# Kernel optimization log

Measured on AMD Instinct MI355X. Metric: run time of the kernel, lower is better.

The kernel has to match this reference:

```python
import jax, jax.numpy as jnp
import numpy as np

S, T, H = 5120, 1024, 512
DL, DT, DC, DU = 512, 32, 64, 64
D = DL + DT + DC  # 608 rnn input size
LOC, TIM, CLU, UID = 50000, 48, 100, 10000


def setup_inputs() -> dict:
    key = jax.random.key(0)
    ks = jax.random.split(key, 20)
    r = lambda k, shape, s=0.02: (jax.random.normal(k, shape, dtype=jnp.float32) * s)
    return {
        "loc": jax.random.randint(ks[0], (S,), 0, LOC),
        "tim": jax.random.randint(ks[1], (S,), 0, TIM),
        "cluster": jax.random.randint(ks[2], (S,), 0, CLU),
        "uid": jax.random.randint(ks[3], (1,), 0, UID),
        "target_len": T,
        "emb_loc": r(ks[4], (LOC, DL)),
        "emb_tim": r(ks[5], (TIM, DT)),
        "emb_cluster": r(ks[6], (CLU, DC)),
        "emb_uid": r(ks[7], (UID, DU)),
        "enc_Wih": r(ks[8], (4 * H, D)),
        "enc_Whh": r(ks[9], (4 * H, H)),
        "enc_bih": jnp.zeros((4 * H,), jnp.float32),
        "enc_bhh": jnp.zeros((4 * H,), jnp.float32),
        "dec_Wih": r(ks[10], (4 * H, D)),
        "dec_Whh": r(ks[11], (4 * H, H)),
        "dec_bih": jnp.zeros((4 * H,), jnp.float32),
        "dec_bhh": jnp.zeros((4 * H,), jnp.float32),
        "fcW": r(ks[12], (LOC, 2 * H + DU)),
        "fcb": jnp.zeros((LOC,), jnp.float32),
    }


def _lstm(x, Wih, Whh, bih, bhh):
    # x: [S, D]; PyTorch LSTM gate order i, f, g, o
    h0 = jnp.zeros((H,), x.dtype)

    def step(carry, xt):
        h, c = carry
        g = xt @ Wih.T + bih + h @ Whh.T + bhh
        i, f, gg, o = jnp.split(g, 4)
        c = jax.nn.sigmoid(f) * c + jax.nn.sigmoid(i) * jnp.tanh(gg)
        h = jax.nn.sigmoid(o) * jnp.tanh(c)
        return (h, c), h

    _, hs = jax.lax.scan(step, (h0, h0), x)
    return hs  # [S, H]


def reference(loc, tim, cluster, uid, target_len, emb_loc, emb_tim, emb_cluster,
              emb_uid, enc_Wih, enc_Whh, enc_bih, enc_bhh, dec_Wih, dec_Whh,
              dec_bih, dec_bhh, fcW, fcb):
    # embed and concat; dropout is identity in eval mode
    x = jnp.concatenate([emb_loc[loc], emb_tim[tim], emb_cluster[cluster]], axis=-1)  # [S, D]
    hidden_history = _lstm(x[:-target_len], enc_Wih, enc_Whh, enc_bih, enc_bhh)  # [S-T, H]
    hidden_state = _lstm(x[-target_len:], dec_Wih, dec_Whh, dec_bih, dec_bhh)   # [T, H]
    # 'dot' attention: the O(T*Sh) python loop of scalar dots == one GEMM
    attn = jax.nn.softmax(hidden_state @ hidden_history.T, axis=-1)  # [T, S-T]
    context = attn @ hidden_history  # [T, H]
    uid_emb = jnp.broadcast_to(emb_uid[uid], (target_len, DU))  # repeat(target_len, 1)
    out = jnp.concatenate([hidden_state, context, uid_emb], axis=1)  # [T, 2H+DU]
    y = out @ fcW.T + fcb  # [T, LOC]
    return jax.nn.log_softmax(y, axis=-1)
```

## Files before the change

kernel.cpp:

```cpp
#include <hip/hip_runtime.h>

typedef unsigned short u16;
typedef unsigned int u32;
typedef unsigned long long u64;
typedef __attribute__((ext_vector_type(8))) short short8;
typedef __attribute__((ext_vector_type(4))) float f32x4;

__device__ __forceinline__ u16 f2bf(float f) {
    u32 u = __float_as_uint(f);
    u32 r = (u + 0x7fffu + ((u >> 16) & 1u)) >> 16;
    return (u16)r;
}
__device__ __forceinline__ float bfl(u32 u) { return __uint_as_float(u << 16); }
__device__ __forceinline__ float bfh(u32 u) { return __uint_as_float(u & 0xffff0000u); }
__device__ __forceinline__ u32 pk2(float a, float b) {
    return (u32)f2bf(a) | ((u32)f2bf(b) << 16);
}

#define S_TOT 5120
#define T_DEC 1024
#define S_ENC 4096
#define HDIM 512
#define DDIM 608
#define G4 2048
#define NLOC 50000
#define KFC 1088

__global__ void k_init(u64* he, u64* hd) {
    int i = blockIdx.x * 256 + threadIdx.x;
    if (i < 512) { he[i] = 0ull; hd[i] = 0ull; }
}

__global__ void k_bias(const float* a, const float* b, const float* c, const float* d,
                       float* be, float* bd) {
    int i = blockIdx.x * 256 + threadIdx.x;
    if (i < G4) { be[i] = a[i] + b[i]; bd[i] = c[i] + d[i]; }
}

__global__ __launch_bounds__(256) void k_embed(const int* __restrict__ loc, const int* __restrict__ tim,
    const int* __restrict__ clu, const float* __restrict__ el, const float* __restrict__ et,
    const float* __restrict__ ec, u16* __restrict__ xb) {
    const int s = blockIdx.x;
    const int ls = loc[s], lt = tim[s], lc = clu[s];
    for (int c = threadIdx.x; c < DDIM; c += 256) {
        float v;
        if (c < 512)       v = el[(size_t)ls * 512 + c];
        else if (c < 544)  v = et[lt * 32 + (c - 512)];
        else               v = ec[lc * 64 + (c - 544)];
        xb[(size_t)s * DDIM + c] = f2bf(v);
    }
}

template <bool BF32>
__global__ __launch_bounds__(256) void gemm_bt(
    const u16* __restrict__ A, const void* __restrict__ Bv, float* __restrict__ C,
    const float* __restrict__ bias, int N, int K, int lda, int ldb, int ldc) {
    __shared__ u16 As[128][40];
    __shared__ u16 Bs[128][40];
    const int tid = threadIdx.x;
    const int bn = blockIdx.x, bm = blockIdx.y;
    const int wave = tid >> 6, lane = tid & 63;
    const int quad = lane >> 4, l16 = lane & 15;
    const int wm = (wave & 1) << 6, wn = (wave >> 1) << 6;
    const int rq = tid >> 2, q4 = tid & 3;

    f32x4 acc[4][4] = {};

    const u16* Arow0 = A + (size_t)(bm * 128 + rq) * lda + q4 * 8;
    const u16* Arow1 = Arow0 + (size_t)64 * lda;

    const int rb0 = bn * 128 + rq, rb1 = rb0 + 64;
    const bool okb0 = rb0 < N, okb1 = rb1 < N;
    const float* Bf0 = nullptr; const float* Bf1 = nullptr;
    const u16* Bh0 = nullptr; const u16* Bh1 = nullptr;
    if constexpr (BF32) {
        const float* Bf = (const float*)Bv;
        Bf0 = Bf + (size_t)rb0 * ldb + q4 * 8;
        Bf1 = Bf + (size_t)rb1 * ldb + q4 * 8;
    } else {
        const u16* Bh = (const u16*)Bv;
        Bh0 = Bh + (size_t)rb0 * ldb + q4 * 8;
        Bh1 = Bh + (size_t)rb1 * ldb + q4 * 8;
    }

    uint4 a0, a1, bh0, bh1;
    float4 f00, f01, f10, f11;
    const float4 fz = make_float4(0.f, 0.f, 0.f, 0.f);
    auto fetch = [&](int k0) {
        a0 = *(const uint4*)(Arow0 + k0);
        a1 = *(const uint4*)(Arow1 + k0);
        if constexpr (BF32) {
            f00 = okb0 ? *(const float4*)(Bf0 + k0) : fz;
            f01 = okb0 ? *(const float4*)(Bf0 + k0 + 4) : fz;
            f10 = okb1 ? *(const float4*)(Bf1 + k0) : fz;
            f11 = okb1 ? *(const float4*)(Bf1 + k0 + 4) : fz;
        } else {
            bh0 = *(const uint4*)(Bh0 + k0);
            bh1 = *(const uint4*)(Bh1 + k0);
        }
    };
    fetch(0);
    for (int k0 = 0; k0 < K; k0 += 32) {
        __syncthreads();
        *(uint4*)&As[rq][q4 * 8] = a0;
        *(uint4*)&As[rq + 64][q4 * 8] = a1;
        if constexpr (BF32) {
            uint4 t0, t1;
            t0.x = pk2(f00.x, f00.y); t0.y = pk2(f00.z, f00.w);
            t0.z = pk2(f01.x, f01.y); t0.w = pk2(f01.z, f01.w);
            t1.x = pk2(f10.x, f10.y); t1.y = pk2(f10.z, f10.w);
            t1.z = pk2(f11.x, f11.y); t1.w = pk2(f11.z, f11.w);
            *(uint4*)&Bs[rq][q4 * 8] = t0;
            *(uint4*)&Bs[rq + 64][q4 * 8] = t1;
        } else {
            *(uint4*)&Bs[rq][q4 * 8] = bh0;
            *(uint4*)&Bs[rq + 64][q4 * 8] = bh1;
        }
        __syncthreads();
        if (k0 + 32 < K) fetch(k0 + 32);
        short8 af[4], bf[4];
#pragma unroll
        for (int i = 0; i < 4; i++) af[i] = *(const short8*)&As[wm + 16 * i + l16][quad * 8];
#pragma unroll
        for (int j = 0; j < 4; j++) bf[j] = *(const short8*)&Bs[wn + 16 * j + l16][quad * 8];
#pragma unroll
        for (int i = 0; i < 4; i++)
#pragma unroll
            for (int j = 0; j < 4; j++)
                acc[i][j] = __builtin_amdgcn_mfma_f32_16x16x32_bf16(af[i], bf[j], acc[i][j], 0, 0, 0);
    }
#pragma unroll
    for (int j = 0; j < 4; j++) {
        int c0 = bn * 128 + wn + 16 * j + l16;
        if (c0 >= N) continue;
        float bv = bias ? bias[c0] : 0.f;
#pragma unroll
        for (int i = 0; i < 4; i++) {
            int r0 = bm * 128 + wm + 16 * i + quad * 4;
#pragma unroll
            for (int rg = 0; rg < 4; rg++)
                C[(size_t)(r0 + rg) * ldc + c0] = acc[i][j][rg] + bv;
        }
    }
}

__global__ __launch_bounds__(256) void k_lstm(
    const float* __restrict__ Whh_e, const float* __restrict__ Whh_d,
    const float* __restrict__ XW,
    u64* __restrict__ hbc_e, u64* __restrict__ hbc_d,
    u16* __restrict__ Hh, u16* __restrict__ HhT, u16* __restrict__ OutA) {
    __shared__ u16 Wl[32][520];
    __shared__ float hbuf[512];
    __shared__ float gbuf[32];
    __shared__ float cbuf[8];
    const int tid = threadIdx.x;
    const bool enc = (blockIdx.x < 64);
    const int w = enc ? blockIdx.x : (blockIdx.x - 64);
    const int steps = enc ? S_ENC : T_DEC;
    const int j0 = w << 3;
    const float* Whh = enc ? Whh_e : Whh_d;
    u64* hbc = enc ? hbc_e : hbc_d;
    const float* XWb = XW + (enc ? (size_t)0 : (size_t)S_ENC * G4);
    const int r = tid >> 3, c8 = tid & 7;
    {
        const int grow = ((r >> 3) << 9) + j0 + (r & 7);
        const float* src = Whh + (size_t)grow * HDIM + c8 * 64;
        u16* dst = &Wl[r][c8 * 64];
        for (int i = 0; i < 64; i += 4) {
            float4 v = *(const float4*)(src + i);
            dst[i] = f2bf(v.x); dst[i + 1] = f2bf(v.y);
            dst[i + 2] = f2bf(v.z); dst[i + 3] = f2bf(v.w);
        }
    }
    if (tid < 8) cbuf[tid] = 0.f;
    const int xw_col = ((r >> 3) << 9) + j0 + (r & 7);
    const int i0 = tid * 2;
    for (int t = 0; t < steps; ++t) {
        float xwv = 0.f;
        if (c8 == 0) xwv = XWb[(size_t)t * G4 + xw_col];
        int dead = 0, spins = 0;
        u64 v0, v1;
        for (;;) {
            v0 = __hip_atomic_load(&hbc[i0], __ATOMIC_RELAXED, __HIP_MEMORY_SCOPE_AGENT);
            v1 = __hip_atomic_load(&hbc[i0 + 1], __ATOMIC_RELAXED, __HIP_MEMORY_SCOPE_AGENT);
            if ((u32)(v0 >> 32) == (u32)t && (u32)(v1 >> 32) == (u32)t) break;
            if (++spins > (1 << 18)) { dead = 1; break; }
        }
        hbuf[i0] = __uint_as_float((u32)v0);
        hbuf[i0 + 1] = __uint_as_float((u32)v1);
        if (__syncthreads_or(dead)) break;
        float acc = 0.f;
        {
            const u16* wr = &Wl[r][c8 * 64];
            const float* hb = &hbuf[c8 * 64];
#pragma unroll
            for (int i = 0; i < 64; i += 8) {
                uint4 wv = *(const uint4*)(wr + i);
                float4 h0 = *(const float4*)(hb + i);
                float4 h1 = *(const float4*)(hb + i + 4);
                acc += bfl(wv.x) * h0.x; acc += bfh(wv.x) * h0.y;
                acc += bfl(wv.y) * h0.z; acc += bfh(wv.y) * h0.w;
                acc += bfl(wv.z) * h1.x; acc += bfh(wv.z) * h1.y;
                acc += bfl(wv.w) * h1.z; acc += bfh(wv.w) * h1.w;
            }
        }
        acc += __shfl_xor(acc, 1);
        acc += __shfl_xor(acc, 2);
        acc += __shfl_xor(acc, 4);
        if (c8 == 0) gbuf[r] = acc + xwv;
        __syncthreads();
        if (tid < 8) {
            const int j = tid;
            float gi = gbuf[j], gf = gbuf[8 + j], gg = gbuf[16 + j], go = gbuf[24 + j];
            float si = 1.f / (1.f + __expf(-gi));
            float sf = 1.f / (1.f + __expf(-gf));
            float so = 1.f / (1.f + __expf(-go));
            float cc = sf * cbuf[j] + si * tanhf(gg);
            cbuf[j] = cc;
            float h = so * tanhf(cc);
            u16 hb16 = f2bf(h);
            if (enc) {
                Hh[(size_t)t * HDIM + j0 + j] = hb16;
                HhT[(size_t)(j0 + j) * S_ENC + t] = hb16;
            } else {
                OutA[(size_t)t * KFC + j0 + j] = hb16;
            }
            u64 pk = ((u64)(u32)(t + 1) << 32) | (u64)__float_as_uint(h);
            __hip_atomic_store(&hbc[j0 + j], pk, __ATOMIC_RELAXED, __HIP_MEMORY_SCOPE_AGENT);
        }
    }
}

__global__ __launch_bounds__(256) void k_softmax(const float* __restrict__ scores, u16* __restrict__ attn) {
    __shared__ float red[8];
    const int t = blockIdx.x, tid = threadIdx.x;
    const float* row = scores + (size_t)t * S_ENC;
    float v[16];
    float m = -3.4e38f;
#pragma unroll
    for (int j = 0; j < 16; ++j) { v[j] = row[tid + 256 * j]; m = fmaxf(m, v[j]); }
    for (int o = 32; o; o >>= 1) m = fmaxf(m, __shfl_xor(m, o));
    if ((tid & 63) == 0) red[tid >> 6] = m;
    __syncthreads();
    m = fmaxf(fmaxf(red[0], red[1]), fmaxf(red[2], red[3]));
    float s = 0.f;
#pragma unroll
    for (int j = 0; j < 16; ++j) { v[j] = __expf(v[j] - m); s += v[j]; }
    for (int o = 32; o; o >>= 1) s += __shfl_xor(s, o);
    if ((tid & 63) == 0) red[4 + (tid >> 6)] = s;
    __syncthreads();
    const float inv = 1.f / (red[4] + red[5] + red[6] + red[7]);
    u16* orow = attn + (size_t)t * S_ENC;
#pragma unroll
    for (int j = 0; j < 16; ++j) orow[tid + 256 * j] = f2bf(v[j] * inv);
}

__global__ void k_finish(const float* __restrict__ ctx, const float* __restrict__ eu,
                         const int* __restrict__ uid, u16* __restrict__ OutA) {
    const int t = blockIdx.x;
    const int u = uid[0];
    for (int c = threadIdx.x; c < 576; c += 256) {
        float v = (c < 512) ? ctx[(size_t)t * 512 + c] : eu[(size_t)u * 64 + (c - 512)];
        OutA[(size_t)t * KFC + 512 + c] = f2bf(v);
    }
}

__global__ __launch_bounds__(256) void k_logsoftmax(float* __restrict__ y) {
    __shared__ float red[8];
    const int t = blockIdx.x, tid = threadIdx.x;
    float* row = y + (size_t)t * NLOC;
    float m = -3.4e38f;
    for (int i = tid; i < NLOC; i += 256) m = fmaxf(m, row[i]);
    for (int o = 32; o; o >>= 1) m = fmaxf(m, __shfl_xor(m, o));
    if ((tid & 63) == 0) red[tid >> 6] = m;
    __syncthreads();
    m = fmaxf(fmaxf(red[0], red[1]), fmaxf(red[2], red[3]));
    float s = 0.f;
    for (int i = tid; i < NLOC; i += 256) s += __expf(row[i] - m);
    for (int o = 32; o; o >>= 1) s += __shfl_xor(s, o);
    if ((tid & 63) == 0) red[4 + (tid >> 6)] = s;
    __syncthreads();
    const float lse = m + __logf(red[4] + red[5] + red[6] + red[7]);
    for (int i = tid; i < NLOC; i += 256) row[i] -= lse;
}

extern "C" void kernel_launch(void* const* d_in, const int* in_sizes, int n_in,
                              void* d_out, int out_size, void* d_ws, size_t ws_size,
                              hipStream_t stream) {
    const int* loc = (const int*)d_in[0];
    const int* tim = (const int*)d_in[1];
    const int* clu = (const int*)d_in[2];
    const int* uid = (const int*)d_in[3];
    const float* emb_loc = (const float*)d_in[5];
    const float* emb_tim = (const float*)d_in[6];
    const float* emb_clu = (const float*)d_in[7];
    const float* emb_uid = (const float*)d_in[8];
    const float* enc_Wih = (const float*)d_in[9];
    const float* enc_Whh = (const float*)d_in[10];
    const float* enc_bih = (const float*)d_in[11];
    const float* enc_bhh = (const float*)d_in[12];
    const float* dec_Wih = (const float*)d_in[13];
    const float* dec_Whh = (const float*)d_in[14];
    const float* dec_bih = (const float*)d_in[15];
    const float* dec_bhh = (const float*)d_in[16];
    const float* fcW = (const float*)d_in[17];
    const float* fcb = (const float*)d_in[18];
    float* out = (float*)d_out;

    char* p = (char*)d_ws;
    auto alloc = [&](size_t bytes) -> void* {
        void* r = (void*)p;
        p += (bytes + 255) & ~(size_t)255;
        return r;
    };
    u16* xb      = (u16*)alloc((size_t)S_TOT * DDIM * 2);
    float* XW    = (float*)alloc((size_t)S_TOT * G4 * 4);
    float* bias_e = (float*)alloc(G4 * 4);
    float* bias_d = (float*)alloc(G4 * 4);
    u64* hbc_e   = (u64*)alloc(512 * 8);
    u64* hbc_d   = (u64*)alloc(512 * 8);
    u16* Hh      = (u16*)alloc((size_t)S_ENC * HDIM * 2);
    u16* HhT     = (u16*)alloc((size_t)HDIM * S_ENC * 2);
    u16* OutA    = (u16*)alloc((size_t)T_DEC * KFC * 2);
    float* scores = (float*)alloc((size_t)T_DEC * S_ENC * 4);
    u16* attn    = (u16*)alloc((size_t)T_DEC * S_ENC * 2);
    float* ctx   = (float*)alloc((size_t)T_DEC * HDIM * 4);

    k_init<<<2, 256, 0, stream>>>(hbc_e, hbc_d);
    k_bias<<<8, 256, 0, stream>>>(enc_bih, enc_bhh, dec_bih, dec_bhh, bias_e, bias_d);
    k_embed<<<S_TOT, 256, 0, stream>>>(loc, tim, clu, emb_loc, emb_tim, emb_clu, xb);
    gemm_bt<true><<<dim3(G4 / 128, S_ENC / 128), 256, 0, stream>>>(
        xb, enc_Wih, XW, bias_e, G4, DDIM, DDIM, DDIM, G4);
    gemm_bt<true><<<dim3(G4 / 128, T_DEC / 128), 256, 0, stream>>>(
        xb + (size_t)S_ENC * DDIM, dec_Wih, XW + (size_t)S_ENC * G4, bias_d, G4, DDIM, DDIM, DDIM, G4);
    k_lstm<<<128, 256, 0, stream>>>(enc_Whh, dec_Whh, XW, hbc_e, hbc_d, Hh, HhT, OutA);
    gemm_bt<false><<<dim3(S_ENC / 128, T_DEC / 128), 256, 0, stream>>>(
        OutA, Hh, scores, nullptr, S_ENC, HDIM, KFC, HDIM, S_ENC);
    k_softmax<<<T_DEC, 256, 0, stream>>>(scores, attn);
    gemm_bt<false><<<dim3(HDIM / 128, T_DEC / 128), 256, 0, stream>>>(
        attn, HhT, ctx, nullptr, HDIM, S_ENC, S_ENC, S_ENC, HDIM);
    k_finish<<<T_DEC, 256, 0, stream>>>(ctx, emb_uid, uid, OutA);
    gemm_bt<true><<<dim3((NLOC + 127) / 128, T_DEC / 128), 256, 0, stream>>>(
        OutA, fcW, out, fcb, NLOC, KFC, KFC, KFC, NLOC);
    k_logsoftmax<<<T_DEC, 256, 0, stream>>>(out);
}
```

Measured before the change: 12.03 ms.

## Restructure LSTM recurrence: packed bf16 hidden exchange, shuffle-based gates, one barrier

The persistent LSTM kernel now exchanges the hidden state as packed bf16 pairs, so each thread polls a single 64-bit flag word instead of two. The rows are reordered so that the four gates of each unit sit in the same wavefront. Gate math then runs through shuffles, which removes the shared-memory gate buffer and the second __syncthreads per step. Fast rcp/exp sigmoid and tanh replace the divisions and tanhf, and h is double-buffered in padded LDS. The cost is that the recurrent input is quantized to bf16, which reduces precision.

```diff
diff --git a/kernel.cpp b/kernel.cpp
--- a/kernel.cpp
+++ b/kernel.cpp
@@ -15,6 +15,12 @@
 __device__ __forceinline__ float bfh(u32 u) { return __uint_as_float(u & 0xffff0000u); }
 __device__ __forceinline__ u32 pk2(float a, float b) {
     return (u32)f2bf(a) | ((u32)f2bf(b) << 16);
+}
+__device__ __forceinline__ float fsig(float x) {
+    return __builtin_amdgcn_rcpf(1.f + __expf(-x));
+}
+__device__ __forceinline__ float ftanh(float x) {
+    return 1.f - 2.f * __builtin_amdgcn_rcpf(1.f + __expf(2.f * x));
 }
 
 #define S_TOT 5120
@@ -28,7 +34,7 @@
 
 __global__ void k_init(u64* he, u64* hd) {
     int i = blockIdx.x * 256 + threadIdx.x;
-    if (i < 512) { he[i] = 0ull; hd[i] = 0ull; }
+    if (i < 256) { he[i] = 0ull; hd[i] = 0ull; }
 }
 
 __global__ void k_bias(const float* a, const float* b, const float* c, const float* d,
@@ -150,9 +156,7 @@
     u64* __restrict__ hbc_e, u64* __restrict__ hbc_d,
     u16* __restrict__ Hh, u16* __restrict__ HhT, u16* __restrict__ OutA) {
     __shared__ u16 Wl[32][520];
-    __shared__ float hbuf[512];
-    __shared__ float gbuf[32];
-    __shared__ float cbuf[8];
+    __shared__ u32 hbuf[2][8 * 33];
     const int tid = threadIdx.x;
     const bool enc = (blockIdx.x < 64);
     const int w = enc ? blockIdx.x : (blockIdx.x - 64);
@@ -162,8 +166,9 @@
     u64* hbc = enc ? hbc_e : hbc_d;
     const float* XWb = XW + (enc ? (size_t)0 : (size_t)S_ENC * G4);
     const int r = tid >> 3, c8 = tid & 7;
+    const int jj = r >> 2, gate = r & 3;
+    const int grow = gate * 512 + j0 + jj;
     {
-        const int grow = ((r >> 3) << 9) + j0 + (r & 7);
         const float* src = Whh + (size_t)grow * HDIM + c8 * 64;
         u16* dst = &Wl[r][c8 * 64];
         for (int i = 0; i < 64; i += 4) {
@@ -172,61 +177,64 @@
             dst[i + 2] = f2bf(v.z); dst[i + 3] = f2bf(v.w);
         }
     }
-    if (tid < 8) cbuf[tid] = 0.f;
-    const int xw_col = ((r >> 3) << 9) + j0 + (r & 7);
-    const int i0 = tid * 2;
+    const int lane = tid & 63;
+    const int wv = tid >> 6;
+    const bool owner = (lane == 0 || lane == 32);
+    const int hoff = (tid >> 5) * 33 + (tid & 31);
+    float c_state = 0.f;
     for (int t = 0; t < steps; ++t) {
-        float xwv = 0.f;
-        if (c8 == 0) xwv = XWb[(size_t)t * G4 + xw_col];
-        int dead = 0, spins = 0;
-        u64 v0, v1;
+        float xwv = XWb[(size_t)t * G4 + grow];
+        int dead = 0; u32 spins = 0; u64 v;
         for (;;) {
-            v0 = __hip_atomic_load(&hbc[i0], __ATOMIC_RELAXED, __HIP_MEMORY_SCOPE_AGENT);
-            v1 = __hip_atomic_load(&hbc[i0 + 1], __ATOMIC_RELAXED, __HIP_MEMORY_SCOPE_AGENT);
-            if ((u32)(v0 >> 32) == (u32)t && (u32)(v1 >> 32) == (u32)t) break;
-            if (++spins > (1 << 18)) { dead = 1; break; }
-        }
-        hbuf[i0] = __uint_as_float((u32)v0);
-        hbuf[i0 + 1] = __uint_as_float((u32)v1);
+            v = __hip_atomic_load(&hbc[tid], __ATOMIC_RELAXED, __HIP_MEMORY_SCOPE_AGENT);
+            if ((u32)(v >> 32) == (u32)t) break;
+            if (++spins > (1u << 19)) { dead = 1; break; }
+        }
+        hbuf[t & 1][hoff] = (u32)v;
         if (__syncthreads_or(dead)) break;
         float acc = 0.f;
         {
             const u16* wr = &Wl[r][c8 * 64];
-            const float* hb = &hbuf[c8 * 64];
-#pragma unroll
-            for (int i = 0; i < 64; i += 8) {
-                uint4 wv = *(const uint4*)(wr + i);
-                float4 h0 = *(const float4*)(hb + i);
-                float4 h1 = *(const float4*)(hb + i + 4);
-                acc += bfl(wv.x) * h0.x; acc += bfh(wv.x) * h0.y;
-                acc += bfl(wv.y) * h0.z; acc += bfh(wv.y) * h0.w;
-                acc += bfl(wv.z) * h1.x; acc += bfh(wv.z) * h1.y;
-                acc += bfl(wv.w) * h1.z; acc += bfh(wv.w) * h1.w;
+            const u32* hb = &hbuf[t & 1][c8 * 33];
+#pragma unroll
+            for (int i = 0; i < 8; i++) {
+                uint4 w4 = *(const uint4*)(wr + i * 8);
+                u32 h0 = hb[i * 4], h1 = hb[i * 4 + 1], h2 = hb[i * 4 + 2], h3 = hb[i * 4 + 3];
+                acc += bfl(w4.x) * bfl(h0); acc += bfh(w4.x) * bfh(h0);
+                acc += bfl(w4.y) * bfl(h1); acc += bfh(w4.y) * bfh(h1);
+                acc += bfl(w4.z) * bfl(h2); acc += bfh(w4.z) * bfh(h2);
+                acc += bfl(w4.w) * bfl(h3); acc += bfh(w4.w) * bfh(h3);
             }
         }
         acc += __shfl_xor(acc, 1);
         acc += __shfl_xor(acc, 2);
         acc += __shfl_xor(acc, 4);
-        if (c8 == 0) gbuf[r] = acc + xwv;
-        __syncthreads();
-        if (tid < 8) {
-            const int j = tid;
-            float gi = gbuf[j], gf = gbuf[8 + j], gg = gbuf[16 + j], go = gbuf[24 + j];
-            float si = 1.f / (1.f + __expf(-gi));
-            float sf = 1.f / (1.f + __expf(-gf));
-            float so = 1.f / (1.f + __expf(-go));
-            float cc = sf * cbuf[j] + si * tanhf(gg);
-            cbuf[j] = cc;
-            float h = so * tanhf(cc);
-            u16 hb16 = f2bf(h);
+        acc += xwv;
+        const int base = lane & 32;
+        float gi = __shfl(acc, base + 0);
+        float gf = __shfl(acc, base + 8);
+        float gg = __shfl(acc, base + 16);
+        float go = __shfl(acc, base + 24);
+        float h = 0.f;
+        if (owner) {
+            float cc = fsig(gf) * c_state + fsig(gi) * ftanh(gg);
+            c_state = cc;
+            h = fsig(go) * ftanh(cc);
+        }
+        float hodd = __shfl(h, 32);
+        if (lane == 0) {
+            const int j = wv * 2;
+            u16 ha = f2bf(h), hb2 = f2bf(hodd);
+            u32 pair = (u32)ha | ((u32)hb2 << 16);
             if (enc) {
-                Hh[(size_t)t * HDIM + j0 + j] = hb16;
-                HhT[(size_t)(j0 + j) * S_ENC + t] = hb16;
+                *(u32*)&Hh[(size_t)t * HDIM + j0 + j] = pair;
+                HhT[(size_t)(j0 + j) * S_ENC + t] = ha;
+                HhT[(size_t)(j0 + j + 1) * S_ENC + t] = hb2;
             } else {
-                OutA[(size_t)t * KFC + j0 + j] = hb16;
+                *(u32*)&OutA[(size_t)t * KFC + j0 + j] = pair;
             }
-            u64 pk = ((u64)(u32)(t + 1) << 32) | (u64)__float_as_uint(h);
-            __hip_atomic_store(&hbc[j0 + j], pk, __ATOMIC_RELAXED, __HIP_MEMORY_SCOPE_AGENT);
+            u64 pk = ((u64)(u32)(t + 1) << 32) | (u64)pair;
+            __hip_atomic_store(&hbc[(j0 >> 1) + wv], pk, __ATOMIC_RELAXED, __HIP_MEMORY_SCOPE_AGENT);
         }
     }
 }
@@ -317,8 +325,8 @@
     float* XW    = (float*)alloc((size_t)S_TOT * G4 * 4);
     float* bias_e = (float*)alloc(G4 * 4);
     float* bias_d = (float*)alloc(G4 * 4);
-    u64* hbc_e   = (u64*)alloc(512 * 8);
-    u64* hbc_d   = (u64*)alloc(512 * 8);
+    u64* hbc_e   = (u64*)alloc(256 * 8);
+    u64* hbc_d   = (u64*)alloc(256 * 8);
     u16* Hh      = (u16*)alloc((size_t)S_ENC * HDIM * 2);
     u16* HhT     = (u16*)alloc((size_t)HDIM * S_ENC * 2);
     u16* OutA    = (u16*)alloc((size_t)T_DEC * KFC * 2);
@@ -326,7 +334,7 @@
     u16* attn    = (u16*)alloc((size_t)T_DEC * S_ENC * 2);
     float* ctx   = (float*)alloc((size_t)T_DEC * HDIM * 4);
 
-    k_init<<<2, 256, 0, stream>>>(hbc_e, hbc_d);
+    k_init<<<1, 256, 0, stream>>>(hbc_e, hbc_d);
     k_bias<<<8, 256, 0, stream>>>(enc_bih, enc_bhh, dec_bih, dec_bhh, bias_e, bias_d);
     k_embed<<<S_TOT, 256, 0, stream>>>(loc, tim, clu, emb_loc, emb_tim, emb_clu, xb);
     gemm_bt<true><<<dim3(G4 / 128, S_ENC / 128), 256, 0, stream>>>(
```

Result: slower. 13.42 ms (+11.5%).
